# Performance work log

Hardware: AMD Instinct MI355X
Metric: run time of the kernel (lower is better)

The kernel has to match this reference:

```python
import jax, jax.numpy as jnp
import numpy as np


def setup_inputs() -> dict:
    key = jax.random.key(0)
    k1, k2, k3, k4 = jax.random.split(key, 4)
    E = 1_600_000
    N = 100_000
    IN, OUT = 128, 256
    edge_index = jax.random.randint(k1, (2, E), 0, N, dtype=jnp.int32)
    time_encoding = jax.random.normal(k2, (E, IN), dtype=jnp.float32)
    # Linear(in_channels, out_channels): weight [OUT, IN], bias [OUT]
    bound = 1.0 / np.sqrt(IN)
    W = jax.random.uniform(k3, (OUT, IN), minval=-bound, maxval=bound, dtype=jnp.float32)
    b = jax.random.uniform(k4, (OUT,), minval=-bound, maxval=bound, dtype=jnp.float32)
    return {"edge_index": edge_index, "time_encoding": time_encoding,
            "num_nodes": N, "W": W, "b": b}


def reference(edge_index, time_encoding, num_nodes, W, b):
    # scatter-add per-edge time encodings into destination-node buckets
    col = edge_index[1]
    agg = jax.ops.segment_sum(time_encoding, col, num_segments=num_nodes)  # [N, IN]
    # dense projection: Linear -> x @ W.T + b
    return agg @ W.T + b  # [N, OUT]
```

## Files before the change

### kernel.cpp

```cpp
#include <hip/hip_runtime.h>

#define IN_CH 128
#define OUT_CH 256
#define NPB 4
#define BLK 256
#define BLK_SCAN 1024

__global__ void zero_i32(int* __restrict__ p, int n) {
  int i = blockIdx.x * blockDim.x + threadIdx.x;
  if (i < n) p[i] = 0;
}

__global__ void hist_kernel(const int* __restrict__ col, int E, int* __restrict__ count) {
  int i = blockIdx.x * blockDim.x + threadIdx.x;
  if (i < E) atomicAdd(&count[col[i]], 1);
}

__global__ void transpose_w(const float* __restrict__ W, float* __restrict__ Wt) {
  int i = blockIdx.x * blockDim.x + threadIdx.x;
  if (i < IN_CH * OUT_CH) {
    int c = i >> 8;
    int t = i & (OUT_CH - 1);
    Wt[i] = W[t * IN_CH + c];
  }
}

__global__ __launch_bounds__(BLK_SCAN) void scan_block_kernel(
    const int* __restrict__ count, int N, int* __restrict__ excl, int* __restrict__ bsum) {
  __shared__ int wsum[16];
  const int tid = threadIdx.x;
  const int i = blockIdx.x * BLK_SCAN + tid;
  const int v = (i < N) ? count[i] : 0;
  int x = v;
#pragma unroll
  for (int d = 1; d < 64; d <<= 1) {
    int t = __shfl_up(x, d, 64);
    if ((tid & 63) >= d) x += t;
  }
  if ((tid & 63) == 63) wsum[tid >> 6] = x;
  __syncthreads();
  if (tid < 16) {
    int s = wsum[tid];
#pragma unroll
    for (int d = 1; d < 16; d <<= 1) {
      int t = __shfl_up(s, d, 16);
      if (tid >= d) s += t;
    }
    wsum[tid] = s;
  }
  __syncthreads();
  const int w = tid >> 6;
  const int prefix = (w == 0) ? 0 : wsum[w - 1];
  if (i < N) excl[i] = prefix + x - v;
  if (tid == BLK_SCAN - 1) bsum[blockIdx.x] = prefix + x;
}

__global__ void scan_bsum_kernel(int* __restrict__ bsum, int nb) {
  __shared__ int tmp[256];
  const int tid = threadIdx.x;
  int run = 0;
  for (int s = 0; s < nb; s += 256) {
    int v = (s + tid < nb) ? bsum[s + tid] : 0;
    tmp[tid] = v;
    __syncthreads();
    for (int d = 1; d < 256; d <<= 1) {
      int t = (tid >= d) ? tmp[tid - d] : 0;
      __syncthreads();
      tmp[tid] += t;
      __syncthreads();
    }
    if (s + tid < nb) bsum[s + tid] = run + tmp[tid] - v;
    run += tmp[255];
    __syncthreads();
  }
}

__global__ void add_offsets_kernel(int* __restrict__ excl, const int* __restrict__ bsum,
                                   int* __restrict__ cursor, int N) {
  int i = blockIdx.x * blockDim.x + threadIdx.x;
  if (i < N) {
    int o = excl[i] + bsum[i / BLK_SCAN];
    excl[i] = o;
    cursor[i] = o;
  }
}

__global__ void scatter_kernel(const int* __restrict__ col, int E,
                               int* __restrict__ cursor, int* __restrict__ sorted) {
  int i = blockIdx.x * blockDim.x + threadIdx.x;
  if (i < E) {
    int c = col[i];
    int pos = atomicAdd(&cursor[c], 1);
    sorted[pos] = i;
  }
}

__global__ __launch_bounds__(BLK) void gather_project_kernel(
    const float* __restrict__ te, const int* __restrict__ offsets,
    const int* __restrict__ cend, const int* __restrict__ sorted,
    const float* __restrict__ Wt, const float* __restrict__ bias,
    float* __restrict__ out, int N) {
  __shared__ float agg[NPB][IN_CH];
  const int g    = threadIdx.x >> 6;
  const int lane = threadIdx.x & 63;
  const int base = blockIdx.x * NPB;
  const int n = base + g;

  float ax = 0.f, ay = 0.f;
  if (n < N) {
    const int s = offsets[n];
    const int e = cend[n];
    if (s < e) {
      const size_t co = (size_t)(lane * 2);
      int my = 0;
      if (lane < 16) {
        int idx = s + lane;
        my = sorted[idx < e ? idx : (e - 1)];
      }
      for (int i = s; i < e; i += 16) {
#define EID(j) __shfl(my, j, 64)
        const float2 t0  = *(const float2*)(te + (size_t)EID(0)  * IN_CH + co);
        const float2 t1  = *(const float2*)(te + (size_t)EID(1)  * IN_CH + co);
        const float2 t2  = *(const float2*)(te + (size_t)EID(2)  * IN_CH + co);
        const float2 t3  = *(const float2*)(te + (size_t)EID(3)  * IN_CH + co);
        const float2 t4  = *(const float2*)(te + (size_t)EID(4)  * IN_CH + co);
        const float2 t5  = *(const float2*)(te + (size_t)EID(5)  * IN_CH + co);
        const float2 t6  = *(const float2*)(te + (size_t)EID(6)  * IN_CH + co);
        const float2 t7  = *(const float2*)(te + (size_t)EID(7)  * IN_CH + co);
        const float2 t8  = *(const float2*)(te + (size_t)EID(8)  * IN_CH + co);
        const float2 t9  = *(const float2*)(te + (size_t)EID(9)  * IN_CH + co);
        const float2 t10 = *(const float2*)(te + (size_t)EID(10) * IN_CH + co);
        const float2 t11 = *(const float2*)(te + (size_t)EID(11) * IN_CH + co);
        const float2 t12 = *(const float2*)(te + (size_t)EID(12) * IN_CH + co);
        const float2 t13 = *(const float2*)(te + (size_t)EID(13) * IN_CH + co);
        const float2 t14 = *(const float2*)(te + (size_t)EID(14) * IN_CH + co);
        const float2 t15 = *(const float2*)(te + (size_t)EID(15) * IN_CH + co);
#undef EID
        int nxt = 0;
        {
          const int ib = i + 16;
          if (lane < 16 && ib < e) {
            int idx = ib + lane;
            nxt = sorted[idx < e ? idx : (e - 1)];
          }
        }
        const int rem = e - i;
        if (rem >= 16) {
          ax += (t0.x + t1.x) + (t2.x + t3.x) + (t4.x + t5.x) + (t6.x + t7.x) +
                (t8.x + t9.x) + (t10.x + t11.x) + (t12.x + t13.x) + (t14.x + t15.x);
          ay += (t0.y + t1.y) + (t2.y + t3.y) + (t4.y + t5.y) + (t6.y + t7.y) +
                (t8.y + t9.y) + (t10.y + t11.y) + (t12.y + t13.y) + (t14.y + t15.y);
        } else {
          ax += t0.x; ay += t0.y;
#define ACC(j, tj) { const float c = (rem > j) ? 1.f : 0.f; \
                     ax = fmaf(c, tj.x, ax); ay = fmaf(c, tj.y, ay); }
          ACC(1, t1)  ACC(2, t2)  ACC(3, t3)  ACC(4, t4)  ACC(5, t5)
          ACC(6, t6)  ACC(7, t7)  ACC(8, t8)  ACC(9, t9)  ACC(10, t10)
          ACC(11, t11) ACC(12, t12) ACC(13, t13) ACC(14, t14) ACC(15, t15)
#undef ACC
        }
        my = nxt;
      }
    }
  }
  {
    float2 r; r.x = ax; r.y = ay;
    *(float2*)(&agg[g][lane * 2]) = r;
  }
  __syncthreads();

  const int t = threadIdx.x;
  float acc[NPB];
#pragma unroll
  for (int gg = 0; gg < NPB; ++gg) acc[gg] = 0.f;
#pragma unroll 8
  for (int c4 = 0; c4 < IN_CH / 4; ++c4) {
    const int c = c4 * 4;
    const float w0 = Wt[(size_t)(c + 0) * OUT_CH + t];
    const float w1 = Wt[(size_t)(c + 1) * OUT_CH + t];
    const float w2 = Wt[(size_t)(c + 2) * OUT_CH + t];
    const float w3 = Wt[(size_t)(c + 3) * OUT_CH + t];
#pragma unroll
    for (int gg = 0; gg < NPB; ++gg) {
      const float4 a = *(const float4*)(&agg[gg][c]);
      acc[gg] = fmaf(w0, a.x, fmaf(w1, a.y, fmaf(w2, a.z, fmaf(w3, a.w, acc[gg]))));
    }
  }
  const float bv = bias[t];
#pragma unroll
  for (int gg = 0; gg < NPB; ++gg) {
    const int nn = base + gg;
    if (nn < N) out[(size_t)nn * OUT_CH + t] = acc[gg] + bv;
  }
}

extern "C" void kernel_launch(void* const* d_in, const int* in_sizes, int n_in,
                              void* d_out, int out_size, void* d_ws, size_t ws_size,
                              hipStream_t stream) {
  const int* edge_index = (const int*)d_in[0];
  const float* te       = (const float*)d_in[1];
  const float* W        = (const float*)d_in[3];
  const float* bias     = (const float*)d_in[4];
  float* out            = (float*)d_out;

  const int E = in_sizes[0] / 2;
  const int N = out_size / OUT_CH;
  const int* col = edge_index + E;

  int* ws      = (int*)d_ws;
  int* count   = ws;
  int* offsets = ws + N;
  int* cursor  = ws + 2 * N;
  int* bsum    = ws + 3 * N;
  int* sorted  = ws + 3 * N + 4096;
  float* Wt    = (float*)(ws + 3 * N + 4096 + E);

  const int nb = (N + BLK_SCAN - 1) / BLK_SCAN;

  hipLaunchKernelGGL(zero_i32, dim3((N + 255) / 256), dim3(256), 0, stream, count, N);
  hipLaunchKernelGGL(transpose_w, dim3((IN_CH * OUT_CH + 255) / 256), dim3(256), 0, stream, W, Wt);
  hipLaunchKernelGGL(hist_kernel, dim3((E + 255) / 256), dim3(256), 0, stream, col, E, count);
  hipLaunchKernelGGL(scan_block_kernel, dim3(nb), dim3(BLK_SCAN), 0, stream, count, N, offsets, bsum);
  hipLaunchKernelGGL(scan_bsum_kernel, dim3(1), dim3(256), 0, stream, bsum, nb);
  hipLaunchKernelGGL(add_offsets_kernel, dim3((N + 255) / 256), dim3(256), 0, stream,
                     offsets, bsum, cursor, N);
  hipLaunchKernelGGL(scatter_kernel, dim3((E + 255) / 256), dim3(256), 0, stream, col, E, cursor, sorted);
  hipLaunchKernelGGL(gather_project_kernel, dim3((N + NPB - 1) / NPB), dim3(BLK), 0, stream,
                     te, offsets, cursor, sorted, Wt, bias, out, N);
}
```

Baseline: 540.4 us.

## Split gather and projection into separate kernels with register-tiled GEMM

Unfuses the per-node gather-sum from the dense projection. Aggregates are written to a global workspace buffer, and a new projection kernel computes 8 nodes by 2 output channels per thread using float2 weight loads. It also merges the count-zeroing and weight-transpose kernels into a single init kernel to save a launch. The aim is to let the gather kernel run without the projection's register and LDS pressure, and to raise FMA reuse per weight load. The cost is an extra round trip of the N×128 aggregate through global memory.

```diff
diff --git a/kernel.cpp b/kernel.cpp
--- a/kernel.cpp
+++ b/kernel.cpp
@@ -2,27 +2,22 @@
 
 #define IN_CH 128
 #define OUT_CH 256
-#define NPB 4
-#define BLK 256
 #define BLK_SCAN 1024
 
-__global__ void zero_i32(int* __restrict__ p, int n) {
-  int i = blockIdx.x * blockDim.x + threadIdx.x;
-  if (i < n) p[i] = 0;
-}
-
-__global__ void hist_kernel(const int* __restrict__ col, int E, int* __restrict__ count) {
-  int i = blockIdx.x * blockDim.x + threadIdx.x;
-  if (i < E) atomicAdd(&count[col[i]], 1);
-}
-
-__global__ void transpose_w(const float* __restrict__ W, float* __restrict__ Wt) {
-  int i = blockIdx.x * blockDim.x + threadIdx.x;
+__global__ void init_kernel(const float* __restrict__ W, float* __restrict__ Wt,
+                            int* __restrict__ count, int N) {
+  int i = blockIdx.x * blockDim.x + threadIdx.x;
+  if (i < N) count[i] = 0;
   if (i < IN_CH * OUT_CH) {
     int c = i >> 8;
     int t = i & (OUT_CH - 1);
     Wt[i] = W[t * IN_CH + c];
   }
+}
+
+__global__ void hist_kernel(const int* __restrict__ col, int E, int* __restrict__ count) {
+  int i = blockIdx.x * blockDim.x + threadIdx.x;
+  if (i < E) atomicAdd(&count[col[i]], 1);
 }
 
 __global__ __launch_bounds__(BLK_SCAN) void scan_block_kernel(
@@ -95,102 +90,126 @@
   }
 }
 
-__global__ __launch_bounds__(BLK) void gather_project_kernel(
+__global__ __launch_bounds__(256) void aggregate_kernel(
     const float* __restrict__ te, const int* __restrict__ offsets,
     const int* __restrict__ cend, const int* __restrict__ sorted,
-    const float* __restrict__ Wt, const float* __restrict__ bias,
-    float* __restrict__ out, int N) {
-  __shared__ float agg[NPB][IN_CH];
+    float* __restrict__ agg, int N) {
   const int g    = threadIdx.x >> 6;
   const int lane = threadIdx.x & 63;
-  const int base = blockIdx.x * NPB;
-  const int n = base + g;
+  const int n = blockIdx.x * 4 + g;
+  if (n >= N) return;
 
   float ax = 0.f, ay = 0.f;
-  if (n < N) {
-    const int s = offsets[n];
-    const int e = cend[n];
-    if (s < e) {
-      const size_t co = (size_t)(lane * 2);
-      int my = 0;
-      if (lane < 16) {
-        int idx = s + lane;
-        my = sorted[idx < e ? idx : (e - 1)];
-      }
-      for (int i = s; i < e; i += 16) {
+  const int s = offsets[n];
+  const int e = cend[n];
+  const size_t co = (size_t)(lane * 2);
+  if (s < e) {
+    int my = 0;
+    if (lane < 16) {
+      int idx = s + lane;
+      my = sorted[idx < e ? idx : (e - 1)];
+    }
+    for (int i = s; i < e; i += 16) {
 #define EID(j) __shfl(my, j, 64)
-        const float2 t0  = *(const float2*)(te + (size_t)EID(0)  * IN_CH + co);
-        const float2 t1  = *(const float2*)(te + (size_t)EID(1)  * IN_CH + co);
-        const float2 t2  = *(const float2*)(te + (size_t)EID(2)  * IN_CH + co);
-        const float2 t3  = *(const float2*)(te + (size_t)EID(3)  * IN_CH + co);
-        const float2 t4  = *(const float2*)(te + (size_t)EID(4)  * IN_CH + co);
-        const float2 t5  = *(const float2*)(te + (size_t)EID(5)  * IN_CH + co);
-        const float2 t6  = *(const float2*)(te + (size_t)EID(6)  * IN_CH + co);
-        const float2 t7  = *(const float2*)(te + (size_t)EID(7)  * IN_CH + co);
-        const float2 t8  = *(const float2*)(te + (size_t)EID(8)  * IN_CH + co);
-        const float2 t9  = *(const float2*)(te + (size_t)EID(9)  * IN_CH + co);
-        const float2 t10 = *(const float2*)(te + (size_t)EID(10) * IN_CH + co);
-        const float2 t11 = *(const float2*)(te + (size_t)EID(11) * IN_CH + co);
-        const float2 t12 = *(const float2*)(te + (size_t)EID(12) * IN_CH + co);
-        const float2 t13 = *(const float2*)(te + (size_t)EID(13) * IN_CH + co);
-        const float2 t14 = *(const float2*)(te + (size_t)EID(14) * IN_CH + co);
-        const float2 t15 = *(const float2*)(te + (size_t)EID(15) * IN_CH + co);
+      const float2 t0  = *(const float2*)(te + (size_t)EID(0)  * IN_CH + co);
+      const float2 t1  = *(const float2*)(te + (size_t)EID(1)  * IN_CH + co);
+      const float2 t2  = *(const float2*)(te + (size_t)EID(2)  * IN_CH + co);
+      const float2 t3  = *(const float2*)(te + (size_t)EID(3)  * IN_CH + co);
+      const float2 t4  = *(const float2*)(te + (size_t)EID(4)  * IN_CH + co);
+      const float2 t5  = *(const float2*)(te + (size_t)EID(5)  * IN_CH + co);
+      const float2 t6  = *(const float2*)(te + (size_t)EID(6)  * IN_CH + co);
+      const float2 t7  = *(const float2*)(te + (size_t)EID(7)  * IN_CH + co);
+      const float2 t8  = *(const float2*)(te + (size_t)EID(8)  * IN_CH + co);
+      const float2 t9  = *(const float2*)(te + (size_t)EID(9)  * IN_CH + co);
+      const float2 t10 = *(const float2*)(te + (size_t)EID(10) * IN_CH + co);
+      const float2 t11 = *(const float2*)(te + (size_t)EID(11) * IN_CH + co);
+      const float2 t12 = *(const float2*)(te + (size_t)EID(12) * IN_CH + co);
+      const float2 t13 = *(const float2*)(te + (size_t)EID(13) * IN_CH + co);
+      const float2 t14 = *(const float2*)(te + (size_t)EID(14) * IN_CH + co);
+      const float2 t15 = *(const float2*)(te + (size_t)EID(15) * IN_CH + co);
 #undef EID
-        int nxt = 0;
-        {
-          const int ib = i + 16;
-          if (lane < 16 && ib < e) {
-            int idx = ib + lane;
-            nxt = sorted[idx < e ? idx : (e - 1)];
-          }
+      int nxt = 0;
+      {
+        const int ib = i + 16;
+        if (lane < 16 && ib < e) {
+          int idx = ib + lane;
+          nxt = sorted[idx < e ? idx : (e - 1)];
         }
-        const int rem = e - i;
-        if (rem >= 16) {
-          ax += (t0.x + t1.x) + (t2.x + t3.x) + (t4.x + t5.x) + (t6.x + t7.x) +
-                (t8.x + t9.x) + (t10.x + t11.x) + (t12.x + t13.x) + (t14.x + t15.x);
-          ay += (t0.y + t1.y) + (t2.y + t3.y) + (t4.y + t5.y) + (t6.y + t7.y) +
-                (t8.y + t9.y) + (t10.y + t11.y) + (t12.y + t13.y) + (t14.y + t15.y);
-        } else {
-          ax += t0.x; ay += t0.y;
+      }
+      const int rem = e - i;
+      if (rem >= 16) {
+        ax += (t0.x + t1.x) + (t2.x + t3.x) + (t4.x + t5.x) + (t6.x + t7.x) +
+              (t8.x + t9.x) + (t10.x + t11.x) + (t12.x + t13.x) + (t14.x + t15.x);
+        ay += (t0.y + t1.y) + (t2.y + t3.y) + (t4.y + t5.y) + (t6.y + t7.y) +
+              (t8.y + t9.y) + (t10.y + t11.y) + (t12.y + t13.y) + (t14.y + t15.y);
+      } else {
+        ax += t0.x; ay += t0.y;
 #define ACC(j, tj) { const float c = (rem > j) ? 1.f : 0.f; \
                      ax = fmaf(c, tj.x, ax); ay = fmaf(c, tj.y, ay); }
-          ACC(1, t1)  ACC(2, t2)  ACC(3, t3)  ACC(4, t4)  ACC(5, t5)
-          ACC(6, t6)  ACC(7, t7)  ACC(8, t8)  ACC(9, t9)  ACC(10, t10)
-          ACC(11, t11) ACC(12, t12) ACC(13, t13) ACC(14, t14) ACC(15, t15)
+        ACC(1, t1)  ACC(2, t2)  ACC(3, t3)  ACC(4, t4)  ACC(5, t5)
+        ACC(6, t6)  ACC(7, t7)  ACC(8, t8)  ACC(9, t9)  ACC(10, t10)
+        ACC(11, t11) ACC(12, t12) ACC(13, t13) ACC(14, t14) ACC(15, t15)
 #undef ACC
-        }
-        my = nxt;
-      }
-    }
-  }
-  {
-    float2 r; r.x = ax; r.y = ay;
-    *(float2*)(&agg[g][lane * 2]) = r;
-  }
-  __syncthreads();
-
-  const int t = threadIdx.x;
-  float acc[NPB];
-#pragma unroll
-  for (int gg = 0; gg < NPB; ++gg) acc[gg] = 0.f;
-#pragma unroll 8
-  for (int c4 = 0; c4 < IN_CH / 4; ++c4) {
-    const int c = c4 * 4;
-    const float w0 = Wt[(size_t)(c + 0) * OUT_CH + t];
-    const float w1 = Wt[(size_t)(c + 1) * OUT_CH + t];
-    const float w2 = Wt[(size_t)(c + 2) * OUT_CH + t];
-    const float w3 = Wt[(size_t)(c + 3) * OUT_CH + t];
-#pragma unroll
-    for (int gg = 0; gg < NPB; ++gg) {
-      const float4 a = *(const float4*)(&agg[gg][c]);
-      acc[gg] = fmaf(w0, a.x, fmaf(w1, a.y, fmaf(w2, a.z, fmaf(w3, a.w, acc[gg]))));
-    }
-  }
-  const float bv = bias[t];
-#pragma unroll
-  for (int gg = 0; gg < NPB; ++gg) {
+      }
+      my = nxt;
+    }
+  }
+  float2 r; r.x = ax; r.y = ay;
+  *(float2*)(agg + (size_t)n * IN_CH + co) = r;
+}
+
+#define PNB 16
+__global__ __launch_bounds__(256) void project_kernel(
+    const float* __restrict__ agg, const float* __restrict__ Wt,
+    const float* __restrict__ bias, float* __restrict__ out, int N) {
+  const int ch2  = threadIdx.x & 127;
+  const int half = threadIdx.x >> 7;
+  const int base = blockIdx.x * PNB + half * 8;
+  float2 acc[8];
+#pragma unroll
+  for (int gg = 0; gg < 8; ++gg) { acc[gg].x = 0.f; acc[gg].y = 0.f; }
+
+  if (base + 8 <= N) {
+#pragma unroll 4
+    for (int c4 = 0; c4 < IN_CH / 4; ++c4) {
+      const int c = c4 * 4;
+      const float2 w0 = *(const float2*)(Wt + (size_t)(c + 0) * OUT_CH + ch2 * 2);
+      const float2 w1 = *(const float2*)(Wt + (size_t)(c + 1) * OUT_CH + ch2 * 2);
+      const float2 w2 = *(const float2*)(Wt + (size_t)(c + 2) * OUT_CH + ch2 * 2);
+      const float2 w3 = *(const float2*)(Wt + (size_t)(c + 3) * OUT_CH + ch2 * 2);
+#pragma unroll
+      for (int gg = 0; gg < 8; ++gg) {
+        const float4 a = *(const float4*)(agg + (size_t)(base + gg) * IN_CH + c);
+        acc[gg].x = fmaf(a.x, w0.x, fmaf(a.y, w1.x, fmaf(a.z, w2.x, fmaf(a.w, w3.x, acc[gg].x))));
+        acc[gg].y = fmaf(a.x, w0.y, fmaf(a.y, w1.y, fmaf(a.z, w2.y, fmaf(a.w, w3.y, acc[gg].y))));
+      }
+    }
+  } else {
+#pragma unroll 4
+    for (int c4 = 0; c4 < IN_CH / 4; ++c4) {
+      const int c = c4 * 4;
+      const float2 w0 = *(const float2*)(Wt + (size_t)(c + 0) * OUT_CH + ch2 * 2);
+      const float2 w1 = *(const float2*)(Wt + (size_t)(c + 1) * OUT_CH + ch2 * 2);
+      const float2 w2 = *(const float2*)(Wt + (size_t)(c + 2) * OUT_CH + ch2 * 2);
+      const float2 w3 = *(const float2*)(Wt + (size_t)(c + 3) * OUT_CH + ch2 * 2);
+#pragma unroll
+      for (int gg = 0; gg < 8; ++gg) {
+        const int nn = (base + gg < N) ? (base + gg) : (N > 0 ? N - 1 : 0);
+        const float4 a = *(const float4*)(agg + (size_t)nn * IN_CH + c);
+        acc[gg].x = fmaf(a.x, w0.x, fmaf(a.y, w1.x, fmaf(a.z, w2.x, fmaf(a.w, w3.x, acc[gg].x))));
+        acc[gg].y = fmaf(a.x, w0.y, fmaf(a.y, w1.y, fmaf(a.z, w2.y, fmaf(a.w, w3.y, acc[gg].y))));
+      }
+    }
+  }
+
+  const float2 bv = *(const float2*)(bias + ch2 * 2);
+#pragma unroll
+  for (int gg = 0; gg < 8; ++gg) {
     const int nn = base + gg;
-    if (nn < N) out[(size_t)nn * OUT_CH + t] = acc[gg] + bv;
+    if (nn < N) {
+      float2 r; r.x = acc[gg].x + bv.x; r.y = acc[gg].y + bv.y;
+      *(float2*)(out + (size_t)nn * OUT_CH + ch2 * 2) = r;
+    }
   }
 }
 
@@ -214,17 +233,21 @@
   int* bsum    = ws + 3 * N;
   int* sorted  = ws + 3 * N + 4096;
   float* Wt    = (float*)(ws + 3 * N + 4096 + E);
+  float* agg   = (float*)(ws + 3 * N + 4096 + E + 32768);
 
   const int nb = (N + BLK_SCAN - 1) / BLK_SCAN;
-
-  hipLaunchKernelGGL(zero_i32, dim3((N + 255) / 256), dim3(256), 0, stream, count, N);
-  hipLaunchKernelGGL(transpose_w, dim3((IN_CH * OUT_CH + 255) / 256), dim3(256), 0, stream, W, Wt);
+  const int init_n = (N > IN_CH * OUT_CH) ? N : IN_CH * OUT_CH;
+
+  hipLaunchKernelGGL(init_kernel, dim3((init_n + 255) / 256), dim3(256), 0, stream,
+                     W, Wt, count, N);
   hipLaunchKernelGGL(hist_kernel, dim3((E + 255) / 256), dim3(256), 0, stream, col, E, count);
   hipLaunchKernelGGL(scan_block_kernel, dim3(nb), dim3(BLK_SCAN), 0, stream, count, N, offsets, bsum);
   hipLaunchKernelGGL(scan_bsum_kernel, dim3(1), dim3(256), 0, stream, bsum, nb);
   hipLaunchKernelGGL(add_offsets_kernel, dim3((N + 255) / 256), dim3(256), 0, stream,
                      offsets, bsum, cursor, N);
   hipLaunchKernelGGL(scatter_kernel, dim3((E + 255) / 256), dim3(256), 0, stream, col, E, cursor, sorted);
-  hipLaunchKernelGGL(gather_project_kernel, dim3((N + NPB - 1) / NPB), dim3(BLK), 0, stream,
-                     te, offsets, cursor, sorted, Wt, bias, out, N);
-}
+  hipLaunchKernelGGL(aggregate_kernel, dim3((N + 3) / 4), dim3(256), 0, stream,
+                     te, offsets, cursor, sorted, agg, N);
+  hipLaunchKernelGGL(project_kernel, dim3((N + PNB - 1) / PNB), dim3(256), 0, stream,
+                     agg, Wt, bias, out, N);
+}
```

Result: slower. 687.6 us (+27.2%).

## Split gather and projection, run projection with bf16 MFMA

Applied to the files above, without the earlier changes.

Splits the fused gather+projection kernel into an aggregation kernel that writes bf16-packed per-node sums and a separate projection kernel using 16x16x32 bf16 MFMA with W prepacked into MFMA fragment layout. Zeroing the counts and packing W are merged into one init kernel. The intent is to move the projection onto matrix cores and out of the bandwidth-bound gather. In exchange it adds a bf16 intermediate round-trip through global memory and bf16 precision loss in both inputs of the matmul. The projection kernel also reads A rows for m up to a multiple of 16 without bounds checks.

```diff
diff --git a/kernel.cpp b/kernel.cpp
--- a/kernel.cpp
+++ b/kernel.cpp
@@ -1,28 +1,39 @@
 #include <hip/hip_runtime.h>
+#include <hip/hip_bf16.h>
 
 #define IN_CH 128
 #define OUT_CH 256
-#define NPB 4
-#define BLK 256
 #define BLK_SCAN 1024
 
-__global__ void zero_i32(int* __restrict__ p, int n) {
-  int i = blockIdx.x * blockDim.x + threadIdx.x;
-  if (i < n) p[i] = 0;
+typedef __bf16 bf16x8 __attribute__((ext_vector_type(8)));
+typedef float f32x4 __attribute__((ext_vector_type(4)));
+
+__device__ inline unsigned short f2bf(float f) {
+  union { float f; unsigned int u; } v; v.f = f;
+  unsigned int u = v.u;
+  u += 0x7FFFu + ((u >> 16) & 1u);
+  return (unsigned short)(u >> 16);
+}
+
+__global__ void init_kernel(const float* __restrict__ W, unsigned short* __restrict__ Bpack,
+                            int* __restrict__ count, int N) {
+  int i = blockIdx.x * blockDim.x + threadIdx.x;
+  if (i < N) count[i] = 0;
+  if (i < IN_CH * OUT_CH) {
+    const int j  = i & 7;
+    const int c  = (i >> 3) & 15;
+    const int kb = (i >> 7) & 3;
+    const int ks = (i >> 9) & 3;
+    const int tn = i >> 11;
+    const int row = tn * 16 + c;
+    const int k   = ks * 32 + kb * 8 + j;
+    Bpack[i] = f2bf(W[(size_t)row * IN_CH + k]);
+  }
 }
 
 __global__ void hist_kernel(const int* __restrict__ col, int E, int* __restrict__ count) {
   int i = blockIdx.x * blockDim.x + threadIdx.x;
   if (i < E) atomicAdd(&count[col[i]], 1);
-}
-
-__global__ void transpose_w(const float* __restrict__ W, float* __restrict__ Wt) {
-  int i = blockIdx.x * blockDim.x + threadIdx.x;
-  if (i < IN_CH * OUT_CH) {
-    int c = i >> 8;
-    int t = i & (OUT_CH - 1);
-    Wt[i] = W[t * IN_CH + c];
-  }
 }
 
 __global__ __launch_bounds__(BLK_SCAN) void scan_block_kernel(
@@ -95,102 +106,111 @@
   }
 }
 
-__global__ __launch_bounds__(BLK) void gather_project_kernel(
+__global__ __launch_bounds__(256) void aggregate_kernel(
     const float* __restrict__ te, const int* __restrict__ offsets,
     const int* __restrict__ cend, const int* __restrict__ sorted,
-    const float* __restrict__ Wt, const float* __restrict__ bias,
-    float* __restrict__ out, int N) {
-  __shared__ float agg[NPB][IN_CH];
+    unsigned int* __restrict__ aggb32, int N) {
   const int g    = threadIdx.x >> 6;
   const int lane = threadIdx.x & 63;
-  const int base = blockIdx.x * NPB;
-  const int n = base + g;
+  const int n = blockIdx.x * 4 + g;
+  if (n >= N) return;
 
   float ax = 0.f, ay = 0.f;
-  if (n < N) {
-    const int s = offsets[n];
-    const int e = cend[n];
-    if (s < e) {
-      const size_t co = (size_t)(lane * 2);
-      int my = 0;
-      if (lane < 16) {
-        int idx = s + lane;
-        my = sorted[idx < e ? idx : (e - 1)];
+  const int s = offsets[n];
+  const int e = cend[n];
+  const size_t co = (size_t)(lane * 2);
+  if (s < e) {
+    int my = 0;
+    if (lane < 16) {
+      int idx = s + lane;
+      my = sorted[idx < e ? idx : (e - 1)];
+    }
+    for (int i = s; i < e; i += 16) {
+#define EID(j) __shfl(my, j, 64)
+      const float2 t0  = *(const float2*)(te + (size_t)EID(0)  * IN_CH + co);
+      const float2 t1  = *(const float2*)(te + (size_t)EID(1)  * IN_CH + co);
+      const float2 t2  = *(const float2*)(te + (size_t)EID(2)  * IN_CH + co);
+      const float2 t3  = *(const float2*)(te + (size_t)EID(3)  * IN_CH + co);
+      const float2 t4  = *(const float2*)(te + (size_t)EID(4)  * IN_CH + co);
+      const float2 t5  = *(const float2*)(te + (size_t)EID(5)  * IN_CH + co);
+      const float2 t6  = *(const float2*)(te + (size_t)EID(6)  * IN_CH + co);
+      const float2 t7  = *(const float2*)(te + (size_t)EID(7)  * IN_CH + co);
+      const float2 t8  = *(const float2*)(te + (size_t)EID(8)  * IN_CH + co);
+      const float2 t9  = *(const float2*)(te + (size_t)EID(9)  * IN_CH + co);
+      const float2 t10 = *(const float2*)(te + (size_t)EID(10) * IN_CH + co);
+      const float2 t11 = *(const float2*)(te + (size_t)EID(11) * IN_CH + co);
+      const float2 t12 = *(const float2*)(te + (size_t)EID(12) * IN_CH + co);
+      const float2 t13 = *(const float2*)(te + (size_t)EID(13) * IN_CH + co);
+      const float2 t14 = *(const float2*)(te + (size_t)EID(14) * IN_CH + co);
+      const float2 t15 = *(const float2*)(te + (size_t)EID(15) * IN_CH + co);
+#undef EID
+      int nxt = 0;
+      {
+        const int ib = i + 16;
+        if (lane < 16 && ib < e) {
+          int idx = ib + lane;
+          nxt = sorted[idx < e ? idx : (e - 1)];
+        }
       }
-      for (int i = s; i < e; i += 16) {
-#define EID(j) __shfl(my, j, 64)
-        const float2 t0  = *(const float2*)(te + (size_t)EID(0)  * IN_CH + co);
-        const float2 t1  = *(const float2*)(te + (size_t)EID(1)  * IN_CH + co);
-        const float2 t2  = *(const float2*)(te + (size_t)EID(2)  * IN_CH + co);
-        const float2 t3  = *(const float2*)(te + (size_t)EID(3)  * IN_CH + co);
-        const float2 t4  = *(const float2*)(te + (size_t)EID(4)  * IN_CH + co);
-        const float2 t5  = *(const float2*)(te + (size_t)EID(5)  * IN_CH + co);
-        const float2 t6  = *(const float2*)(te + (size_t)EID(6)  * IN_CH + co);
-        const float2 t7  = *(const float2*)(te + (size_t)EID(7)  * IN_CH + co);
-        const float2 t8  = *(const float2*)(te + (size_t)EID(8)  * IN_CH + co);
-        const float2 t9  = *(const float2*)(te + (size_t)EID(9)  * IN_CH + co);
-        const float2 t10 = *(const float2*)(te + (size_t)EID(10) * IN_CH + co);
-        const float2 t11 = *(const float2*)(te + (size_t)EID(11) * IN_CH + co);
-        const float2 t12 = *(const float2*)(te + (size_t)EID(12) * IN_CH + co);
-        const float2 t13 = *(const float2*)(te + (size_t)EID(13) * IN_CH + co);
-        const float2 t14 = *(const float2*)(te + (size_t)EID(14) * IN_CH + co);
-        const float2 t15 = *(const float2*)(te + (size_t)EID(15) * IN_CH + co);
-#undef EID
-        int nxt = 0;
-        {
-          const int ib = i + 16;
-          if (lane < 16 && ib < e) {
-            int idx = ib + lane;
-            nxt = sorted[idx < e ? idx : (e - 1)];
-          }
-        }
-        const int rem = e - i;
-        if (rem >= 16) {
-          ax += (t0.x + t1.x) + (t2.x + t3.x) + (t4.x + t5.x) + (t6.x + t7.x) +
-                (t8.x + t9.x) + (t10.x + t11.x) + (t12.x + t13.x) + (t14.x + t15.x);
-          ay += (t0.y + t1.y) + (t2.y + t3.y) + (t4.y + t5.y) + (t6.y + t7.y) +
-                (t8.y + t9.y) + (t10.y + t11.y) + (t12.y + t13.y) + (t14.y + t15.y);
-        } else {
-          ax += t0.x; ay += t0.y;
+      const int rem = e - i;
+      if (rem >= 16) {
+        ax += (t0.x + t1.x) + (t2.x + t3.x) + (t4.x + t5.x) + (t6.x + t7.x) +
+              (t8.x + t9.x) + (t10.x + t11.x) + (t12.x + t13.x) + (t14.x + t15.x);
+        ay += (t0.y + t1.y) + (t2.y + t3.y) + (t4.y + t5.y) + (t6.y + t7.y) +
+              (t8.y + t9.y) + (t10.y + t11.y) + (t12.y + t13.y) + (t14.y + t15.y);
+      } else {
+        ax += t0.x; ay += t0.y;
 #define ACC(j, tj) { const float c = (rem > j) ? 1.f : 0.f; \
                      ax = fmaf(c, tj.x, ax); ay = fmaf(c, tj.y, ay); }
-          ACC(1, t1)  ACC(2, t2)  ACC(3, t3)  ACC(4, t4)  ACC(5, t5)
-          ACC(6, t6)  ACC(7, t7)  ACC(8, t8)  ACC(9, t9)  ACC(10, t10)
-          ACC(11, t11) ACC(12, t12) ACC(13, t13) ACC(14, t14) ACC(15, t15)
+        ACC(1, t1)  ACC(2, t2)  ACC(3, t3)  ACC(4, t4)  ACC(5, t5)
+        ACC(6, t6)  ACC(7, t7)  ACC(8, t8)  ACC(9, t9)  ACC(10, t10)
+        ACC(11, t11) ACC(12, t12) ACC(13, t13) ACC(14, t14) ACC(15, t15)
 #undef ACC
-        }
-        my = nxt;
       }
-    }
-  }
-  {
-    float2 r; r.x = ax; r.y = ay;
-    *(float2*)(&agg[g][lane * 2]) = r;
-  }
-  __syncthreads();
-
-  const int t = threadIdx.x;
-  float acc[NPB];
-#pragma unroll
-  for (int gg = 0; gg < NPB; ++gg) acc[gg] = 0.f;
-#pragma unroll 8
-  for (int c4 = 0; c4 < IN_CH / 4; ++c4) {
-    const int c = c4 * 4;
-    const float w0 = Wt[(size_t)(c + 0) * OUT_CH + t];
-    const float w1 = Wt[(size_t)(c + 1) * OUT_CH + t];
-    const float w2 = Wt[(size_t)(c + 2) * OUT_CH + t];
-    const float w3 = Wt[(size_t)(c + 3) * OUT_CH + t];
-#pragma unroll
-    for (int gg = 0; gg < NPB; ++gg) {
-      const float4 a = *(const float4*)(&agg[gg][c]);
-      acc[gg] = fmaf(w0, a.x, fmaf(w1, a.y, fmaf(w2, a.z, fmaf(w3, a.w, acc[gg]))));
-    }
-  }
-  const float bv = bias[t];
-#pragma unroll
-  for (int gg = 0; gg < NPB; ++gg) {
-    const int nn = base + gg;
-    if (nn < N) out[(size_t)nn * OUT_CH + t] = acc[gg] + bv;
+      my = nxt;
+    }
+  }
+  aggb32[(size_t)n * 64 + lane] = (unsigned int)f2bf(ax) | ((unsigned int)f2bf(ay) << 16);
+}
+
+__global__ __launch_bounds__(256) void project_mfma(
+    const unsigned short* __restrict__ aggb, const unsigned short* __restrict__ Bpack,
+    const float* __restrict__ bias, float* __restrict__ out, int N) {
+  const int wave = threadIdx.x >> 6;
+  const int lane = threadIdx.x & 63;
+  const int r  = lane & 15;
+  const int kb = lane >> 4;
+  const int m0 = blockIdx.x * 16;
+
+  bf16x8 a[4];
+  const unsigned short* arow = aggb + (size_t)(m0 + r) * IN_CH + kb * 8;
+#pragma unroll
+  for (int ks = 0; ks < 4; ++ks)
+    a[ks] = *(const bf16x8*)(arow + ks * 32);
+
+  f32x4 acc[4];
+#pragma unroll
+  for (int ct = 0; ct < 4; ++ct) acc[ct] = (f32x4){0.f, 0.f, 0.f, 0.f};
+
+#pragma unroll
+  for (int ct = 0; ct < 4; ++ct) {
+    const int tn = wave * 4 + ct;
+#pragma unroll
+    for (int ks = 0; ks < 4; ++ks) {
+      const bf16x8 b = *(const bf16x8*)(Bpack + (size_t)((((tn * 4 + ks) * 4 + kb) * 16 + r) * 8));
+      acc[ct] = __builtin_amdgcn_mfma_f32_16x16x32_bf16(a[ks], b, acc[ct], 0, 0, 0);
+    }
+  }
+
+#pragma unroll
+  for (int ct = 0; ct < 4; ++ct) {
+    const int col = wave * 64 + ct * 16 + r;
+    const float bv = bias[col];
+#pragma unroll
+    for (int j = 0; j < 4; ++j) {
+      const int m = m0 + kb * 4 + j;
+      if (m < N) out[(size_t)m * OUT_CH + col] = acc[ct][j] + bv;
+    }
   }
 }
 
@@ -207,24 +227,30 @@
   const int N = out_size / OUT_CH;
   const int* col = edge_index + E;
 
+  const int Np = (N + 3) & ~3;
+  const int Ep = (E + 3) & ~3;
   int* ws      = (int*)d_ws;
   int* count   = ws;
-  int* offsets = ws + N;
-  int* cursor  = ws + 2 * N;
-  int* bsum    = ws + 3 * N;
-  int* sorted  = ws + 3 * N + 4096;
-  float* Wt    = (float*)(ws + 3 * N + 4096 + E);
+  int* offsets = ws + Np;
+  int* cursor  = ws + 2 * Np;
+  int* bsum    = ws + 3 * Np;
+  int* sorted  = ws + 3 * Np + 4096;
+  unsigned short* Bpack = (unsigned short*)(ws + 3 * Np + 4096 + Ep);
+  unsigned int*   aggb  = (unsigned int*)(ws + 3 * Np + 4096 + Ep + 16384);
 
   const int nb = (N + BLK_SCAN - 1) / BLK_SCAN;
-
-  hipLaunchKernelGGL(zero_i32, dim3((N + 255) / 256), dim3(256), 0, stream, count, N);
-  hipLaunchKernelGGL(transpose_w, dim3((IN_CH * OUT_CH + 255) / 256), dim3(256), 0, stream, W, Wt);
+  const int init_n = (N > IN_CH * OUT_CH) ? N : IN_CH * OUT_CH;
+
+  hipLaunchKernelGGL(init_kernel, dim3((init_n + 255) / 256), dim3(256), 0, stream,
+                     W, Bpack, count, N);
   hipLaunchKernelGGL(hist_kernel, dim3((E + 255) / 256), dim3(256), 0, stream, col, E, count);
   hipLaunchKernelGGL(scan_block_kernel, dim3(nb), dim3(BLK_SCAN), 0, stream, count, N, offsets, bsum);
   hipLaunchKernelGGL(scan_bsum_kernel, dim3(1), dim3(256), 0, stream, bsum, nb);
   hipLaunchKernelGGL(add_offsets_kernel, dim3((N + 255) / 256), dim3(256), 0, stream,
                      offsets, bsum, cursor, N);
   hipLaunchKernelGGL(scatter_kernel, dim3((E + 255) / 256), dim3(256), 0, stream, col, E, cursor, sorted);
-  hipLaunchKernelGGL(gather_project_kernel, dim3((N + NPB - 1) / NPB), dim3(BLK), 0, stream,
-                     te, offsets, cursor, sorted, Wt, bias, out, N);
-}
+  hipLaunchKernelGGL(aggregate_kernel, dim3((N + 3) / 4), dim3(256), 0, stream,
+                     te, offsets, cursor, sorted, aggb, N);
+  hipLaunchKernelGGL(project_mfma, dim3((N + 15) / 16), dim3(256), 0, stream,
+                     (const unsigned short*)aggb, Bpack, bias, out, N);
+}
```

Result: faster. 448.6 us (-17.0%).
